# Kernel tuning notes

Measured on AMD Instinct MI355X. Metric: run time of the kernel, lower is better.

Reference implementation:

```python
import jax, jax.numpy as jnp
import numpy as np

N_NODES = 100000
N_EDGES = 1600000


def _lin_init(k, din, dout):
    # xavier-normal-ish weight, zero bias handled separately
    s = (2.0 / (din + dout)) ** 0.5
    return jax.random.normal(k, (din, dout), jnp.float32) * s


def setup_inputs() -> dict:
    key = jax.random.key(0)
    ks = jax.random.split(key, 32)
    inp = {
        "node_feat": jax.random.normal(ks[0], (N_NODES, 3), jnp.float32),
        "edge_feat": jax.random.normal(ks[1], (N_EDGES, 1), jnp.float32),
        "edge_dist": jax.random.normal(ks[2], (N_EDGES, 1), jnp.float32),
        "src": jax.random.randint(ks[3], (N_EDGES,), 0, N_NODES),
        "dst": jax.random.randint(ks[4], (N_EDGES,), 0, N_NODES),
    }
    dims = {"enc": [3, 64, 64, 8], "dec": [8, 64, 64, 1],
            "nod": [9, 64, 64, 8], "edg": [17, 64, 64, 1]}
    i = 5
    for name, d in dims.items():
        for l in range(3):
            inp[f"w_{name}{l+1}"] = _lin_init(ks[i], d[l], d[l + 1]); i += 1
            inp[f"b_{name}{l+1}"] = jnp.zeros((d[l + 1],), jnp.float32)
    return inp


def _mlp(x, w1, b1, w2, b2, w3, b3):
    x = jax.nn.relu(x @ w1 + b1)
    x = jax.nn.relu(x @ w2 + b2)
    return jax.nn.relu(x @ w3 + b3)


def _edge_softmax(dist, dst, n):
    # softmax over incoming edges per destination node (DGL edge_softmax)
    m = jax.ops.segment_max(dist, dst, num_segments=n)          # [N,1]
    e = jnp.exp(dist - m[dst])                                   # [E,1]
    s = jax.ops.segment_sum(e, dst, num_segments=n)              # [N,1]
    return e / s[dst]


def reference(node_feat, edge_feat, edge_dist, src, dst,
              w_enc1, b_enc1, w_enc2, b_enc2, w_enc3, b_enc3,
              w_dec1, b_dec1, w_dec2, b_dec2, w_dec3, b_dec3,
              w_nod1, b_nod1, w_nod2, b_nod2, w_nod3, b_nod3,
              w_edg1, b_edg1, w_edg2, b_edg2, w_edg3, b_edg3):
    n = node_feat.shape[0]
    # encoder: [N,3] -> [N,8]
    h = _mlp(node_feat, w_enc1, b_enc1, w_enc2, b_enc2, w_enc3, b_enc3)
    # softmax-weighted aggregation of src features to dst
    w = _edge_softmax(edge_dist, dst, n)                         # [E,1]
    h = jax.ops.segment_sum(w * h[src], dst, num_segments=n)     # [N,8]
    he = edge_feat                                               # [E,1]
    for _ in range(2):
        x = jnp.concatenate([he, h[src], h[dst]], axis=-1)       # [E,17]
        he = _mlp(x, w_edg1, b_edg1, w_edg2, b_edg2, w_edg3, b_edg3)  # [E,1]
        agg = jax.ops.segment_sum(he, dst, num_segments=n)       # [N,1]
        h = _mlp(jnp.concatenate([agg, h], axis=-1),
                 w_nod1, b_nod1, w_nod2, b_nod2, w_nod3, b_nod3)  # [N,8]
    # second softmax aggregation (same dist -> same weights)
    h = jax.ops.segment_sum(w * h[src], dst, num_segments=n)     # [N,8]
    # decoder: [N,8] -> [N,1]
    return _mlp(h, w_dec1, b_dec1, w_dec2, b_dec2, w_dec3, b_dec3)
```

## Files before the change

### kernel.cpp

```cpp
#include <hip/hip_runtime.h>

#define N_NODES 100000
#define N_EDGES 1600000


__global__ void zero_kernel(float* p, int n) {
    int i = blockIdx.x * blockDim.x + threadIdx.x;
    int stride = gridDim.x * blockDim.x;
    for (; i < n; i += stride) p[i] = 0.f;
}

__global__ void seg_max_kernel(const float* __restrict__ dist, const int* __restrict__ dst,
                               unsigned* __restrict__ m, int E) {
    int e = blockIdx.x * blockDim.x + threadIdx.x;
    if (e >= E) return;
    unsigned raw = __float_as_uint(dist[e]);
    unsigned mono = (raw & 0x80000000u) ? ~raw : (raw | 0x80000000u);
    atomicMax(m + dst[e], mono);
}

__global__ void exp_sum_kernel(const float* __restrict__ dist, const int* __restrict__ dst,
                               const unsigned* __restrict__ m, float* __restrict__ s,
                               float* __restrict__ wbuf, int E) {
    int e = blockIdx.x * blockDim.x + threadIdx.x;
    if (e >= E) return;
    int d = dst[e];
    unsigned mono = m[d];
    unsigned raw = (mono & 0x80000000u) ? (mono & 0x7FFFFFFFu) : ~mono;
    float mx = __uint_as_float(raw);
    float v = expf(dist[e] - mx);
    wbuf[e] = v;
    atomicAdd(s + d, v);
}

template <bool NORM>
__global__ void agg_kernel(float* wbuf, const float* __restrict__ s,
                           const float* __restrict__ hfeat,
                           const int* __restrict__ src, const int* __restrict__ dst,
                           float* __restrict__ out, int E) {
    int t = blockIdx.x * blockDim.x + threadIdx.x;
    if (t >= E * 8) return;
    int e = t >> 3, c = t & 7;
    float w = wbuf[e];
    int d = dst[e];
    if (NORM) {
        w = w / s[d];
        if (c == 0) wbuf[e] = w;
    }
    atomicAdd(out + d * 8 + c, w * hfeat[src[e] * 8 + c]);
}

struct PackArgs { const float *w1, *b1, *w2; float* out; int din, stride; };

__global__ void pack_kernel(PackArgs a0, PackArgs a1, PackArgs a2, PackArgs a3) {
    PackArgs a = (blockIdx.x == 0) ? a0 : (blockIdx.x == 1) ? a1
               : (blockIdx.x == 2) ? a2 : a3;
    int k = threadIdx.x;
    float* row = a.out + k * a.stride;
    for (int j = 0; j < 64; ++j) row[j] = a.w2[k * 64 + j];
    for (int j = 0; j < a.din; ++j) row[64 + j] = a.w1[j * 64 + k];
    row[64 + a.din] = a.b1[k];
}

template <int DIN, int DOUT, int STRIDE>
__device__ __forceinline__ void mlp_fused(
    const float* __restrict__ x, const float* __restrict__ wp,
    const float* __restrict__ b2,
    const float* __restrict__ w3, const float* __restrict__ b3,
    float* __restrict__ out) {
    float h2[64];
#pragma unroll
    for (int j = 0; j < 64; ++j) h2[j] = b2[j];
    for (int k = 0; k < 64; ++k) {
        const float* row = wp + k * STRIDE;
        float a = row[64 + DIN];
#pragma unroll
        for (int j = 0; j < DIN; ++j) a = fmaf(x[j], row[64 + j], a);
        a = fmaxf(a, 0.f);
#pragma unroll
        for (int j = 0; j < 64; ++j) h2[j] = fmaf(a, row[j], h2[j]);
    }
    float acc[DOUT];
#pragma unroll
    for (int o = 0; o < DOUT; ++o) acc[o] = b3[o];
#pragma unroll
    for (int j = 0; j < 64; ++j) {
        float r = fmaxf(h2[j], 0.f);
#pragma unroll
        for (int o = 0; o < DOUT; ++o) acc[o] = fmaf(r, w3[j * DOUT + o], acc[o]);
    }
#pragma unroll
    for (int o = 0; o < DOUT; ++o) out[o] = fmaxf(acc[o], 0.f);
}

template <int CA, int CB, int DOUT, int STRIDE>
__global__ __launch_bounds__(256, 4) void node_mlp_kernel(
    const float* __restrict__ xa, const float* __restrict__ xb,
    const float* __restrict__ wp, const float* __restrict__ b2,
    const float* __restrict__ w3, const float* __restrict__ b3,
    float* __restrict__ out, int n) {
    constexpr int DIN = CA + CB;
    int i = blockIdx.x * 256 + threadIdx.x;
    if (i >= n) return;
    float x[DIN];
#pragma unroll
    for (int k = 0; k < CA; ++k) x[k] = xa[i * CA + k];
    if (CB == 8) {
        float4 v0 = *(const float4*)(xb + i * 8);
        float4 v1 = *(const float4*)(xb + i * 8 + 4);
        x[CA + 0] = v0.x; x[CA + 1] = v0.y; x[CA + 2] = v0.z; x[CA + 3] = v0.w;
        x[CA + 4] = v1.x; x[CA + 5] = v1.y; x[CA + 6] = v1.z; x[CA + 7] = v1.w;
    }
    float o[DOUT];
    mlp_fused<DIN, DOUT, STRIDE>(x, wp, b2, w3, b3, o);
#pragma unroll
    for (int k = 0; k < DOUT; ++k) out[i * DOUT + k] = o[k];
}

__global__ __launch_bounds__(256, 4) void edge_mlp_kernel(
    const float* __restrict__ he_in, const float* __restrict__ h,
    const int* __restrict__ src, const int* __restrict__ dst,
    const float* __restrict__ wp, const float* __restrict__ b2,
    const float* __restrict__ w3, const float* __restrict__ b3,
    float* __restrict__ he_out, float* __restrict__ agg, int E) {
    int e = blockIdx.x * 256 + threadIdx.x;
    if (e >= E) return;
    int d = dst[e], sr = src[e];
    float x[17];
    x[0] = he_in[e];
    float4 a0 = *(const float4*)(h + sr * 8);
    float4 a1 = *(const float4*)(h + sr * 8 + 4);
    float4 d0 = *(const float4*)(h + d * 8);
    float4 d1 = *(const float4*)(h + d * 8 + 4);
    x[1] = a0.x;  x[2] = a0.y;  x[3] = a0.z;  x[4] = a0.w;
    x[5] = a1.x;  x[6] = a1.y;  x[7] = a1.z;  x[8] = a1.w;
    x[9] = d0.x;  x[10] = d0.y; x[11] = d0.z; x[12] = d0.w;
    x[13] = d1.x; x[14] = d1.y; x[15] = d1.z; x[16] = d1.w;
    float o;
    mlp_fused<17, 1, 96>(x, wp, b2, w3, b3, &o);
    he_out[e] = o;
    atomicAdd(agg + d, o);
}

extern "C" void kernel_launch(void* const* d_in, const int* in_sizes, int n_in,
                              void* d_out, int out_size, void* d_ws, size_t ws_size,
                              hipStream_t stream) {
    const int N = N_NODES, E = N_EDGES;
    const float* node_feat = (const float*)d_in[0];
    const float* edge_feat = (const float*)d_in[1];
    const float* edge_dist = (const float*)d_in[2];
    const int* src = (const int*)d_in[3];
    const int* dst = (const int*)d_in[4];
    const float* w_enc1 = (const float*)d_in[5];  const float* b_enc1 = (const float*)d_in[6];
    const float* w_enc2 = (const float*)d_in[7];  const float* b_enc2 = (const float*)d_in[8];
    const float* w_enc3 = (const float*)d_in[9];  const float* b_enc3 = (const float*)d_in[10];
    const float* w_dec1 = (const float*)d_in[11]; const float* b_dec1 = (const float*)d_in[12];
    const float* w_dec2 = (const float*)d_in[13]; const float* b_dec2 = (const float*)d_in[14];
    const float* w_dec3 = (const float*)d_in[15]; const float* b_dec3 = (const float*)d_in[16];
    const float* w_nod1 = (const float*)d_in[17]; const float* b_nod1 = (const float*)d_in[18];
    const float* w_nod2 = (const float*)d_in[19]; const float* b_nod2 = (const float*)d_in[20];
    const float* w_nod3 = (const float*)d_in[21]; const float* b_nod3 = (const float*)d_in[22];
    const float* w_edg1 = (const float*)d_in[23]; const float* b_edg1 = (const float*)d_in[24];
    const float* w_edg2 = (const float*)d_in[25]; const float* b_edg2 = (const float*)d_in[26];
    const float* w_edg3 = (const float*)d_in[27]; const float* b_edg3 = (const float*)d_in[28];

    float* ws = (float*)d_ws;
    unsigned* m   = (unsigned*)ws;
    float* s      = ws + N;
    float* hagg1  = ws + 2 * N;
    float* agg1   = ws + 10 * N;
    float* agg2   = ws + 11 * N;
    float* hagg2  = ws + 12 * N;
    float* h_enc  = ws + 20 * N;
    float* h_r1   = ws + 28 * N;
    float* h_r2   = ws + 36 * N;
    float* wbuf   = ws + 44 * N;
    float* he1    = wbuf + E;
    float* he2    = he1 + E;
    float* pk_enc = he2 + E;
    float* pk_nod = pk_enc + 64 * 80;
    float* pk_edg = pk_nod + 64 * 80;
    float* pk_dec = pk_edg + 64 * 96;

    PackArgs pa0{w_enc1, b_enc1, w_enc2, pk_enc, 3, 80};
    PackArgs pa1{w_nod1, b_nod1, w_nod2, pk_nod, 9, 80};
    PackArgs pa2{w_edg1, b_edg1, w_edg2, pk_edg, 17, 96};
    PackArgs pa3{w_dec1, b_dec1, w_dec2, pk_dec, 8, 80};
    pack_kernel<<<4, 64, 0, stream>>>(pa0, pa1, pa2, pa3);

    zero_kernel<<<2048, 256, 0, stream>>>(ws, 20 * N);
    node_mlp_kernel<3, 0, 8, 80><<<(N + 255) / 256, 256, 0, stream>>>(node_feat, nullptr,
        pk_enc, b_enc2, w_enc3, b_enc3, h_enc, N);
    seg_max_kernel<<<(E + 255) / 256, 256, 0, stream>>>(edge_dist, dst, m, E);
    exp_sum_kernel<<<(E + 255) / 256, 256, 0, stream>>>(edge_dist, dst, m, s, wbuf, E);
    agg_kernel<true><<<(E * 8 + 255) / 256, 256, 0, stream>>>(wbuf, s, h_enc, src, dst, hagg1, E);
    edge_mlp_kernel<<<(E + 255) / 256, 256, 0, stream>>>(edge_feat, hagg1, src, dst,
        pk_edg, b_edg2, w_edg3, b_edg3, he1, agg1, E);
    node_mlp_kernel<1, 8, 8, 80><<<(N + 255) / 256, 256, 0, stream>>>(agg1, hagg1,
        pk_nod, b_nod2, w_nod3, b_nod3, h_r1, N);
    edge_mlp_kernel<<<(E + 255) / 256, 256, 0, stream>>>(he1, h_r1, src, dst,
        pk_edg, b_edg2, w_edg3, b_edg3, he2, agg2, E);
    node_mlp_kernel<1, 8, 8, 80><<<(N + 255) / 256, 256, 0, stream>>>(agg2, h_r1,
        pk_nod, b_nod2, w_nod3, b_nod3, h_r2, N);
    agg_kernel<false><<<(E * 8 + 255) / 256, 256, 0, stream>>>(wbuf, s, h_r2, src, dst, hagg2, E);
    node_mlp_kernel<8, 0, 1, 80><<<(N + 255) / 256, 256, 0, stream>>>(hagg2, nullptr,
        pk_dec, b_dec2, w_dec3, b_dec3, (float*)d_out, N);
}
```

Measured before the change: 896.5 us.

## Build CSR by destination and replace atomic scatters with per-node gathers

Builds a destination-sorted CSR (count, scan, fill) at runtime, then computes edge softmax, weighted aggregation and the edge-output sum as per-node gathers instead of float atomics. The edge MLP now processes two edges per thread so each weight load is shared, which raises register pressure, and the launch-bounds occupancy hint is dropped. The CSR build adds several small kernels plus atomic-based fill, and gathers over irregular degree lists may have load imbalance.

```diff
diff --git a/kernel.cpp b/kernel.cpp
--- a/kernel.cpp
+++ b/kernel.cpp
@@ -2,52 +2,105 @@
 
 #define N_NODES 100000
 #define N_EDGES 1600000
-
-
-__global__ void zero_kernel(float* p, int n) {
+#define E_HALF  (N_EDGES / 2)
+
+__global__ void zero_int_kernel(int* p, int n) {
     int i = blockIdx.x * blockDim.x + threadIdx.x;
-    int stride = gridDim.x * blockDim.x;
-    for (; i < n; i += stride) p[i] = 0.f;
-}
-
-__global__ void seg_max_kernel(const float* __restrict__ dist, const int* __restrict__ dst,
-                               unsigned* __restrict__ m, int E) {
+    if (i < n) p[i] = 0;
+}
+
+__global__ void count_kernel(const int* __restrict__ dst, int* __restrict__ cnt, int E) {
+    int e = blockIdx.x * blockDim.x + threadIdx.x;
+    if (e < E) atomicAdd(cnt + dst[e], 1);
+}
+
+__global__ void scan1_kernel(const int* __restrict__ cnt, int* __restrict__ off,
+                             int* __restrict__ bsum, int n) {
+    __shared__ int s[256];
+    int i = blockIdx.x * 256 + threadIdx.x;
+    int v = (i < n) ? cnt[i] : 0;
+    s[threadIdx.x] = v;
+    __syncthreads();
+    for (int o = 1; o < 256; o <<= 1) {
+        int t = (threadIdx.x >= o) ? s[threadIdx.x - o] : 0;
+        __syncthreads();
+        s[threadIdx.x] += t;
+        __syncthreads();
+    }
+    if (i < n) off[i] = s[threadIdx.x] - v;
+    if (threadIdx.x == 255) bsum[blockIdx.x] = s[255];
+}
+
+__global__ void scan2_kernel(const int* __restrict__ bsum, int* __restrict__ boff, int nb) {
+    __shared__ int s[512];
+    int v = (threadIdx.x < nb) ? bsum[threadIdx.x] : 0;
+    s[threadIdx.x] = v;
+    __syncthreads();
+    for (int o = 1; o < 512; o <<= 1) {
+        int t = (threadIdx.x >= o) ? s[threadIdx.x - o] : 0;
+        __syncthreads();
+        s[threadIdx.x] += t;
+        __syncthreads();
+    }
+    if (threadIdx.x < nb) boff[threadIdx.x] = s[threadIdx.x] - v;
+}
+
+__global__ void scan3_kernel(int* __restrict__ off, const int* __restrict__ boff,
+                             int* __restrict__ cursor, int n, int E) {
+    int i = blockIdx.x * 256 + threadIdx.x;
+    if (i < n) {
+        int v = off[i] + boff[blockIdx.x];
+        off[i] = v;
+        cursor[i] = v;
+    }
+    if (i == 0) off[n] = E;
+}
+
+__global__ void fill_kernel(const int* __restrict__ dst, int* __restrict__ cursor,
+                            int* __restrict__ col, int E) {
     int e = blockIdx.x * blockDim.x + threadIdx.x;
     if (e >= E) return;
-    unsigned raw = __float_as_uint(dist[e]);
-    unsigned mono = (raw & 0x80000000u) ? ~raw : (raw | 0x80000000u);
-    atomicMax(m + dst[e], mono);
-}
-
-__global__ void exp_sum_kernel(const float* __restrict__ dist, const int* __restrict__ dst,
-                               const unsigned* __restrict__ m, float* __restrict__ s,
-                               float* __restrict__ wbuf, int E) {
-    int e = blockIdx.x * blockDim.x + threadIdx.x;
-    if (e >= E) return;
-    int d = dst[e];
-    unsigned mono = m[d];
-    unsigned raw = (mono & 0x80000000u) ? (mono & 0x7FFFFFFFu) : ~mono;
-    float mx = __uint_as_float(raw);
-    float v = expf(dist[e] - mx);
-    wbuf[e] = v;
-    atomicAdd(s + d, v);
-}
-
-template <bool NORM>
-__global__ void agg_kernel(float* wbuf, const float* __restrict__ s,
-                           const float* __restrict__ hfeat,
-                           const int* __restrict__ src, const int* __restrict__ dst,
-                           float* __restrict__ out, int E) {
-    int t = blockIdx.x * blockDim.x + threadIdx.x;
-    if (t >= E * 8) return;
-    int e = t >> 3, c = t & 7;
-    float w = wbuf[e];
-    int d = dst[e];
-    if (NORM) {
-        w = w / s[d];
-        if (c == 0) wbuf[e] = w;
-    }
-    atomicAdd(out + d * 8 + c, w * hfeat[src[e] * 8 + c]);
+    int p = atomicAdd(cursor + dst[e], 1);
+    col[p] = e;
+}
+
+__global__ void softmax_kernel(const float* __restrict__ dist,
+                               const int* __restrict__ off, const int* __restrict__ col,
+                               float* __restrict__ wnorm, int N) {
+    int t = blockIdx.x * 256 + threadIdx.x;
+    if (t >= N * 8) return;
+    int d = t >> 3, l = t & 7;
+    int beg = off[d], deg = off[d + 1] - beg;
+    float m = -3.4e38f;
+    for (int i = l; i < deg; i += 8) m = fmaxf(m, dist[col[beg + i]]);
+    m = fmaxf(m, __shfl_xor(m, 1));
+    m = fmaxf(m, __shfl_xor(m, 2));
+    m = fmaxf(m, __shfl_xor(m, 4));
+    float s = 0.f;
+    for (int i = l; i < deg; i += 8) s += expf(dist[col[beg + i]] - m);
+    s += __shfl_xor(s, 1);
+    s += __shfl_xor(s, 2);
+    s += __shfl_xor(s, 4);
+    for (int i = l; i < deg; i += 8) {
+        int e = col[beg + i];
+        wnorm[e] = expf(dist[e] - m) / s;
+    }
+}
+
+__global__ void wsum_kernel(const float* __restrict__ w, const float* __restrict__ h,
+                            const int* __restrict__ src,
+                            const int* __restrict__ off, const int* __restrict__ col,
+                            float* __restrict__ out, int N) {
+    int t = blockIdx.x * 256 + threadIdx.x;
+    if (t >= N * 8) return;
+    int d = t >> 3, c = t & 7;
+    int beg = off[d], deg = off[d + 1] - beg;
+    float acc = 0.f;
+    for (int i = 0; i < deg; ++i) {
+        int e = col[beg + i];
+        acc = fmaf(w[e], h[src[e] * 8 + c], acc);
+    }
+    out[d * 8 + c] = acc;
 }
 
 struct PackArgs { const float *w1, *b1, *w2; float* out; int din, stride; };
@@ -93,53 +146,110 @@
     for (int o = 0; o < DOUT; ++o) out[o] = fmaxf(acc[o], 0.f);
 }
 
-template <int CA, int CB, int DOUT, int STRIDE>
+template <int CA, int DOUT, int STRIDE>
 __global__ __launch_bounds__(256, 4) void node_mlp_kernel(
-    const float* __restrict__ xa, const float* __restrict__ xb,
+    const float* __restrict__ xa,
     const float* __restrict__ wp, const float* __restrict__ b2,
     const float* __restrict__ w3, const float* __restrict__ b3,
     float* __restrict__ out, int n) {
-    constexpr int DIN = CA + CB;
     int i = blockIdx.x * 256 + threadIdx.x;
     if (i >= n) return;
-    float x[DIN];
+    float x[CA];
 #pragma unroll
     for (int k = 0; k < CA; ++k) x[k] = xa[i * CA + k];
-    if (CB == 8) {
-        float4 v0 = *(const float4*)(xb + i * 8);
-        float4 v1 = *(const float4*)(xb + i * 8 + 4);
-        x[CA + 0] = v0.x; x[CA + 1] = v0.y; x[CA + 2] = v0.z; x[CA + 3] = v0.w;
-        x[CA + 4] = v1.x; x[CA + 5] = v1.y; x[CA + 6] = v1.z; x[CA + 7] = v1.w;
-    }
     float o[DOUT];
-    mlp_fused<DIN, DOUT, STRIDE>(x, wp, b2, w3, b3, o);
+    mlp_fused<CA, DOUT, STRIDE>(x, wp, b2, w3, b3, o);
 #pragma unroll
     for (int k = 0; k < DOUT; ++k) out[i * DOUT + k] = o[k];
 }
 
-__global__ __launch_bounds__(256, 4) void edge_mlp_kernel(
+__global__ __launch_bounds__(256, 4) void node_mlp_gather_kernel(
+    const float* __restrict__ he, const float* __restrict__ hprev,
+    const int* __restrict__ off, const int* __restrict__ col,
+    const float* __restrict__ wp, const float* __restrict__ b2,
+    const float* __restrict__ w3, const float* __restrict__ b3,
+    float* __restrict__ out, int n) {
+    int d = blockIdx.x * 256 + threadIdx.x;
+    if (d >= n) return;
+    int beg = off[d], deg = off[d + 1] - beg;
+    float agg = 0.f;
+    for (int i = 0; i < deg; ++i) agg += he[col[beg + i]];
+    float x[9];
+    x[0] = agg;
+    float4 v0 = *(const float4*)(hprev + d * 8);
+    float4 v1 = *(const float4*)(hprev + d * 8 + 4);
+    x[1] = v0.x; x[2] = v0.y; x[3] = v0.z; x[4] = v0.w;
+    x[5] = v1.x; x[6] = v1.y; x[7] = v1.z; x[8] = v1.w;
+    float o[8];
+    mlp_fused<9, 8, 80>(x, wp, b2, w3, b3, o);
+#pragma unroll
+    for (int k = 0; k < 8; ++k) out[d * 8 + k] = o[k];
+}
+
+__global__ __launch_bounds__(256) void edge_mlp2_kernel(
     const float* __restrict__ he_in, const float* __restrict__ h,
     const int* __restrict__ src, const int* __restrict__ dst,
     const float* __restrict__ wp, const float* __restrict__ b2,
     const float* __restrict__ w3, const float* __restrict__ b3,
-    float* __restrict__ he_out, float* __restrict__ agg, int E) {
-    int e = blockIdx.x * 256 + threadIdx.x;
-    if (e >= E) return;
-    int d = dst[e], sr = src[e];
-    float x[17];
-    x[0] = he_in[e];
-    float4 a0 = *(const float4*)(h + sr * 8);
-    float4 a1 = *(const float4*)(h + sr * 8 + 4);
-    float4 d0 = *(const float4*)(h + d * 8);
-    float4 d1 = *(const float4*)(h + d * 8 + 4);
-    x[1] = a0.x;  x[2] = a0.y;  x[3] = a0.z;  x[4] = a0.w;
-    x[5] = a1.x;  x[6] = a1.y;  x[7] = a1.z;  x[8] = a1.w;
-    x[9] = d0.x;  x[10] = d0.y; x[11] = d0.z; x[12] = d0.w;
-    x[13] = d1.x; x[14] = d1.y; x[15] = d1.z; x[16] = d1.w;
-    float o;
-    mlp_fused<17, 1, 96>(x, wp, b2, w3, b3, &o);
-    he_out[e] = o;
-    atomicAdd(agg + d, o);
+    float* __restrict__ he_out) {
+    int t = blockIdx.x * 256 + threadIdx.x;
+    if (t >= E_HALF) return;
+    int e0 = t, e1 = t + E_HALF;
+    float x0[17], x1[17];
+    {
+        int d = dst[e0], sr = src[e0];
+        x0[0] = he_in[e0];
+        float4 a0 = *(const float4*)(h + sr * 8);
+        float4 a1 = *(const float4*)(h + sr * 8 + 4);
+        float4 d0 = *(const float4*)(h + d * 8);
+        float4 d1 = *(const float4*)(h + d * 8 + 4);
+        x0[1] = a0.x;  x0[2] = a0.y;  x0[3] = a0.z;  x0[4] = a0.w;
+        x0[5] = a1.x;  x0[6] = a1.y;  x0[7] = a1.z;  x0[8] = a1.w;
+        x0[9] = d0.x;  x0[10] = d0.y; x0[11] = d0.z; x0[12] = d0.w;
+        x0[13] = d1.x; x0[14] = d1.y; x0[15] = d1.z; x0[16] = d1.w;
+    }
+    {
+        int d = dst[e1], sr = src[e1];
+        x1[0] = he_in[e1];
+        float4 a0 = *(const float4*)(h + sr * 8);
+        float4 a1 = *(const float4*)(h + sr * 8 + 4);
+        float4 d0 = *(const float4*)(h + d * 8);
+        float4 d1 = *(const float4*)(h + d * 8 + 4);
+        x1[1] = a0.x;  x1[2] = a0.y;  x1[3] = a0.z;  x1[4] = a0.w;
+        x1[5] = a1.x;  x1[6] = a1.y;  x1[7] = a1.z;  x1[8] = a1.w;
+        x1[9] = d0.x;  x1[10] = d0.y; x1[11] = d0.z; x1[12] = d0.w;
+        x1[13] = d1.x; x1[14] = d1.y; x1[15] = d1.z; x1[16] = d1.w;
+    }
+    float h2a[64], h2b[64];
+#pragma unroll
+    for (int j = 0; j < 64; ++j) { h2a[j] = b2[j]; h2b[j] = b2[j]; }
+    for (int k = 0; k < 64; ++k) {
+        const float* row = wp + k * 96;
+        float a0 = row[64 + 17], a1 = row[64 + 17];
+#pragma unroll
+        for (int j = 0; j < 17; ++j) {
+            float wv = row[64 + j];
+            a0 = fmaf(x0[j], wv, a0);
+            a1 = fmaf(x1[j], wv, a1);
+        }
+        a0 = fmaxf(a0, 0.f);
+        a1 = fmaxf(a1, 0.f);
+#pragma unroll
+        for (int j = 0; j < 64; ++j) {
+            float wv = row[j];
+            h2a[j] = fmaf(a0, wv, h2a[j]);
+            h2b[j] = fmaf(a1, wv, h2b[j]);
+        }
+    }
+    float acc0 = b3[0], acc1 = b3[0];
+#pragma unroll
+    for (int j = 0; j < 64; ++j) {
+        float wv = w3[j];
+        acc0 = fmaf(fmaxf(h2a[j], 0.f), wv, acc0);
+        acc1 = fmaf(fmaxf(h2b[j], 0.f), wv, acc1);
+    }
+    he_out[e0] = fmaxf(acc0, 0.f);
+    he_out[e1] = fmaxf(acc1, 0.f);
 }
 
 extern "C" void kernel_launch(void* const* d_in, const int* in_sizes, int n_in,
@@ -164,23 +274,28 @@
     const float* w_edg2 = (const float*)d_in[25]; const float* b_edg2 = (const float*)d_in[26];
     const float* w_edg3 = (const float*)d_in[27]; const float* b_edg3 = (const float*)d_in[28];
 
-    float* ws = (float*)d_ws;
-    unsigned* m   = (unsigned*)ws;
-    float* s      = ws + N;
-    float* hagg1  = ws + 2 * N;
-    float* agg1   = ws + 10 * N;
-    float* agg2   = ws + 11 * N;
-    float* hagg2  = ws + 12 * N;
-    float* h_enc  = ws + 20 * N;
-    float* h_r1   = ws + 28 * N;
-    float* h_r2   = ws + 36 * N;
-    float* wbuf   = ws + 44 * N;
-    float* he1    = wbuf + E;
-    float* he2    = he1 + E;
-    float* pk_enc = he2 + E;
+    int* cnt  = (int*)d_ws;
+    int* off  = cnt + N;
+    int* col  = off + N + 8;
+    int* bsum = col + E;
+    int* boff = bsum + 512;
+    float* wnorm = (float*)(boff + 512);
+    float* he1   = wnorm + E;
+    float* he2   = he1 + E;
+    float* hagg1 = he2 + E;
+    float* hagg2 = hagg1 + 8 * N;
+    float* h_enc = hagg2 + 8 * N;
+    float* h_r1  = h_enc + 8 * N;
+    float* h_r2  = h_r1 + 8 * N;
+    float* pk_enc = h_r2 + 8 * N;
     float* pk_nod = pk_enc + 64 * 80;
     float* pk_edg = pk_nod + 64 * 80;
     float* pk_dec = pk_edg + 64 * 96;
+
+    const int NB = (N + 255) / 256;
+    const int EB = (E + 255) / 256;
+    const int GB = (N * 8 + 255) / 256;
+    const int HB = (E_HALF + 255) / 256;
 
     PackArgs pa0{w_enc1, b_enc1, w_enc2, pk_enc, 3, 80};
     PackArgs pa1{w_nod1, b_nod1, w_nod2, pk_nod, 9, 80};
@@ -188,21 +303,26 @@
     PackArgs pa3{w_dec1, b_dec1, w_dec2, pk_dec, 8, 80};
     pack_kernel<<<4, 64, 0, stream>>>(pa0, pa1, pa2, pa3);
 
-    zero_kernel<<<2048, 256, 0, stream>>>(ws, 20 * N);
-    node_mlp_kernel<3, 0, 8, 80><<<(N + 255) / 256, 256, 0, stream>>>(node_feat, nullptr,
+    zero_int_kernel<<<NB, 256, 0, stream>>>(cnt, N);
+    count_kernel<<<EB, 256, 0, stream>>>(dst, cnt, E);
+    scan1_kernel<<<NB, 256, 0, stream>>>(cnt, off, bsum, N);
+    scan2_kernel<<<1, 512, 0, stream>>>(bsum, boff, NB);
+    scan3_kernel<<<NB, 256, 0, stream>>>(off, boff, cnt, N, E);
+    fill_kernel<<<EB, 256, 0, stream>>>(dst, cnt, col, E);
+
+    node_mlp_kernel<3, 8, 80><<<NB, 256, 0, stream>>>(node_feat,
         pk_enc, b_enc2, w_enc3, b_enc3, h_enc, N);
-    seg_max_kernel<<<(E + 255) / 256, 256, 0, stream>>>(edge_dist, dst, m, E);
-    exp_sum_kernel<<<(E + 255) / 256, 256, 0, stream>>>(edge_dist, dst, m, s, wbuf, E);
-    agg_kernel<true><<<(E * 8 + 255) / 256, 256, 0, stream>>>(wbuf, s, h_enc, src, dst, hagg1, E);
-    edge_mlp_kernel<<<(E + 255) / 256, 256, 0, stream>>>(edge_feat, hagg1, src, dst,
-        pk_edg, b_edg2, w_edg3, b_edg3, he1, agg1, E);
-    node_mlp_kernel<1, 8, 8, 80><<<(N + 255) / 256, 256, 0, stream>>>(agg1, hagg1,
+    softmax_kernel<<<GB, 256, 0, stream>>>(edge_dist, off, col, wnorm, N);
+    wsum_kernel<<<GB, 256, 0, stream>>>(wnorm, h_enc, src, off, col, hagg1, N);
+    edge_mlp2_kernel<<<HB, 256, 0, stream>>>(edge_feat, hagg1, src, dst,
+        pk_edg, b_edg2, w_edg3, b_edg3, he1);
+    node_mlp_gather_kernel<<<NB, 256, 0, stream>>>(he1, hagg1, off, col,
         pk_nod, b_nod2, w_nod3, b_nod3, h_r1, N);
-    edge_mlp_kernel<<<(E + 255) / 256, 256, 0, stream>>>(he1, h_r1, src, dst,
-        pk_edg, b_edg2, w_edg3, b_edg3, he2, agg2, E);
-    node_mlp_kernel<1, 8, 8, 80><<<(N + 255) / 256, 256, 0, stream>>>(agg2, h_r1,
+    edge_mlp2_kernel<<<HB, 256, 0, stream>>>(he1, h_r1, src, dst,
+        pk_edg, b_edg2, w_edg3, b_edg3, he2);
+    node_mlp_gather_kernel<<<NB, 256, 0, stream>>>(he2, h_r1, off, col,
         pk_nod, b_nod2, w_nod3, b_nod3, h_r2, N);
-    agg_kernel<false><<<(E * 8 + 255) / 256, 256, 0, stream>>>(wbuf, s, h_r2, src, dst, hagg2, E);
-    node_mlp_kernel<8, 0, 1, 80><<<(N + 255) / 256, 256, 0, stream>>>(hagg2, nullptr,
+    wsum_kernel<<<GB, 256, 0, stream>>>(wnorm, h_r2, src, off, col, hagg2, N);
+    node_mlp_kernel<8, 1, 80><<<NB, 256, 0, stream>>>(hagg2,
         pk_dec, b_dec2, w_dec3, b_dec3, (float*)d_out, N);
 }
```

New measurement: 1.028 ms. 1.15x slower.
